# Optimization experiments

Measured on AMD Instinct MI355X. Metric: run time of the kernel, lower is better.

## Reference

```python
import jax, jax.numpy as jnp
import numpy as np
import math

PAD = 0
EPS = 1e-5


def _mha(x, ids, num_heads, qw, qb, kw, kb, vw, vb, pw, pb):
    # Faithful vectorization of the per-head Python loop: identical math per head.
    B, S, D = x.shape
    d = D // num_heads
    q = (x @ qw + qb).reshape(B, S, num_heads, d)
    k = (x @ kw + kb).reshape(B, S, num_heads, d)
    v = (x @ vw + vb).reshape(B, S, num_heads, d)
    scores = jnp.einsum('bqhd,bkhd->bhqk', q, k) / math.sqrt(d)
    key_mask = (ids != PAD)[:, None, None, :]  # mask padded KEYS only (as in source)
    scores = jnp.where(key_mask, scores, -jnp.inf)
    w = jax.nn.softmax(scores, axis=-1)
    out = jnp.einsum('bhqk,bkhd->bqhd', w, v).reshape(B, S, D)
    return out @ pw + pb + x  # projection + residual


def setup_inputs() -> dict:
    V, D, B, S = 50257, 1024, 64, 512
    key = jax.random.key(0)
    ks = jax.random.split(key, 24)
    s = 0.02

    def lin(k, din, dout):
        k1, k2 = jax.random.split(k)
        return (jax.random.normal(k1, (din, dout), jnp.float32) * s,
                jax.random.normal(k2, (dout,), jnp.float32) * s)

    x = jax.random.randint(ks[0], (B, S), 0, V, dtype=jnp.int64)
    emb_w = jax.random.normal(ks[1], (V, D), jnp.float32) * s
    pos_w = jax.random.normal(ks[2], (512, D), jnp.float32) * s
    a1_qw, a1_qb = lin(ks[3], D, D)
    a1_kw, a1_kb = lin(ks[4], D, D)
    a1_vw, a1_vb = lin(ks[5], D, D)
    a1_pw, a1_pb = lin(ks[6], D, D)
    a2_qw, a2_qb = lin(ks[7], D, D)
    a2_kw, a2_kb = lin(ks[8], D, D)
    a2_vw, a2_vb = lin(ks[9], D, D)
    a2_pw, a2_pb = lin(ks[10], D, D)
    norm_g = jnp.ones((D,), jnp.float32)
    norm_b = jnp.zeros((D,), jnp.float32)
    lin_w, lin_b = lin(ks[11], D, 1)
    return dict(x=x, emb_w=emb_w, pos_w=pos_w,
                a1_qw=a1_qw, a1_qb=a1_qb, a1_kw=a1_kw, a1_kb=a1_kb,
                a1_vw=a1_vw, a1_vb=a1_vb, a1_pw=a1_pw, a1_pb=a1_pb,
                a2_qw=a2_qw, a2_qb=a2_qb, a2_kw=a2_kw, a2_kb=a2_kb,
                a2_vw=a2_vw, a2_vb=a2_vb, a2_pw=a2_pw, a2_pb=a2_pb,
                norm_g=norm_g, norm_b=norm_b, lin_w=lin_w, lin_b=lin_b)


def reference(x, emb_w, pos_w,
              a1_qw, a1_qb, a1_kw, a1_kb, a1_vw, a1_vb, a1_pw, a1_pb,
              a2_qw, a2_qb, a2_kw, a2_kb, a2_vw, a2_vb, a2_pw, a2_pb,
              norm_g, norm_b, lin_w, lin_b):
    B, S = x.shape
    h = emb_w[x] + pos_w[jnp.arange(S)][None, :, :]  # word + positional emb
    res_emb = h
    h = _mha(h, x, 8, a1_qw, a1_qb, a1_kw, a1_kb, a1_vw, a1_vb, a1_pw, a1_pb)
    # dropout is identity in eval
    h = _mha(h, x, 4, a2_qw, a2_qb, a2_kw, a2_kb, a2_vw, a2_vb, a2_pw, a2_pb)
    h = h + res_emb
    # mean pooling over non-pad tokens (type=0 branch)
    m = (x != PAD)[:, :, None].astype(h.dtype)
    pooled = jnp.sum(h * m, axis=1) / jnp.sum(m, axis=1)
    # LayerNorm
    mu = jnp.mean(pooled, axis=-1, keepdims=True)
    var = jnp.mean((pooled - mu) ** 2, axis=-1, keepdims=True)
    normed = (pooled - mu) / jnp.sqrt(var + EPS) * norm_g + norm_b
    return normed @ lin_w + lin_b  # [B, 1]
```

## Files before the change

kernel.cpp:

```cpp
#include <hip/hip_runtime.h>

typedef unsigned short u16;
typedef short short8 __attribute__((ext_vector_type(8)));
typedef unsigned short u16x8 __attribute__((ext_vector_type(8)));
typedef float f32x4 __attribute__((ext_vector_type(4)));
typedef const __attribute__((address_space(1))) void* gptr_t;
typedef __attribute__((address_space(3))) void* lptr_t;

#define B_  64
#define S_  512
#define D_  1024
#define BS_ (B_*S_)

__device__ __forceinline__ float b2f(u16 v) {
    union { float f; unsigned u; } c; c.u = ((unsigned)v) << 16; return c.f;
}
__device__ __forceinline__ u16 f2b(float f) {
    union { float f; unsigned u; } c; c.f = f;
    unsigned r = c.u + 0x7FFFu + ((c.u >> 16) & 1u);
    return (u16)(r >> 16);
}

__global__ void detect_k(const u16* __restrict__ raw, int* __restrict__ flag) {
    __shared__ int cnt;
    if (threadIdx.x == 0) cnt = 0;
    __syncthreads();
    u16 v = raw[threadIdx.x * 2];
    int e = (v >> 7) & 0xFF;
    int sane = (e >= 64 && e <= 150) ? 1 : 0;
    atomicAdd(&cnt, sane);
    __syncthreads();
    if (threadIdx.x == 0) *flag = (cnt >= 192) ? 1 : 0;
}

__global__ __launch_bounds__(256) void convert_params_k(
    const void* b0, const void* b1, const void* b2, const void* b3,
    const void* b4, const void* b5, const void* b6, const void* b7,
    const void* g, const void* be, const void* lw, const void* lb,
    const int* __restrict__ flagp, u16* __restrict__ dst)
{
    const void* srcs[12] = {b0, b1, b2, b3, b4, b5, b6, b7, g, be, lw, lb};
    int slot = blockIdx.x;
    int n = (slot == 11) ? 1 : 1024;
    int f = *flagp;
    const void* s = srcs[slot];
    for (int i = threadIdx.x; i < n; i += 256) {
        float v = f ? b2f(((const u16*)s)[i]) : ((const float*)s)[i];
        dst[slot * 1024 + i] = f2b(v);
    }
}

__global__ __launch_bounds__(256) void transpose_k(const void* __restrict__ W,
                                                   u16* __restrict__ Wt,
                                                   const int* __restrict__ flagp) {
    __shared__ float t[32][33];
    int f = *flagp;
    int tx = threadIdx.x, ty = threadIdx.y;
    int x0 = blockIdx.x * 32, y0 = blockIdx.y * 32;
    for (int i = ty; i < 32; i += 8) {
        size_t idx = (size_t)(y0 + i) * D_ + x0 + tx;
        t[i][tx] = f ? b2f(((const u16*)W)[idx]) : ((const float*)W)[idx];
    }
    __syncthreads();
    for (int i = ty; i < 32; i += 8)
        Wt[(size_t)(x0 + i) * D_ + y0 + tx] = f2b(t[tx][i]);
}

__global__ __launch_bounds__(256) void embed_k(const int* __restrict__ x, const void* __restrict__ emb,
                                               const void* __restrict__ pos, u16* __restrict__ h0,
                                               const int* __restrict__ flagp) {
    int f = *flagp;
    int bs = blockIdx.x;
    int s = bs & (S_ - 1);
    int tok = x[bs];
    u16* orow = h0 + (size_t)bs * D_;
    int c = threadIdx.x * 4;
    float e0, e1, e2, e3, p0, p1, p2, p3;
    if (f) {
        ushort4 e = *(const ushort4*)((const u16*)emb + (size_t)tok * D_ + c);
        ushort4 p = *(const ushort4*)((const u16*)pos + (size_t)s * D_ + c);
        e0 = b2f(e.x); e1 = b2f(e.y); e2 = b2f(e.z); e3 = b2f(e.w);
        p0 = b2f(p.x); p1 = b2f(p.y); p2 = b2f(p.z); p3 = b2f(p.w);
    } else {
        float4 e = *(const float4*)((const float*)emb + (size_t)tok * D_ + c);
        float4 p = *(const float4*)((const float*)pos + (size_t)s * D_ + c);
        e0 = e.x; e1 = e.y; e2 = e.z; e3 = e.w;
        p0 = p.x; p1 = p.y; p2 = p.z; p3 = p.w;
    }
    ushort4 o;
    o.x = f2b(e0 + p0); o.y = f2b(e1 + p1); o.z = f2b(e2 + p2); o.w = f2b(e3 + p3);
    *(ushort4*)(orow + c) = o;
}

template <int NT>
__global__ __launch_bounds__(512, 2) void gemm256_k(
    const u16* __restrict__ A, const u16* __restrict__ Bt,
    const u16* __restrict__ bias,
    const u16* __restrict__ res, const u16* __restrict__ res2,
    u16* __restrict__ Cq, u16* __restrict__ Ck, u16* __restrict__ Vt)
{
    int bid = blockIdx.x;
    int xcd = bid & 7;
    int loc = bid >> 3;
    int chunk = loc >> 6;
    int r = loc & 63;
    int mt = xcd * 16 + (r >> 2);
    int nt = chunk * 4 + (r & 3);
    int m0 = mt * 256, n0 = nt * 256;

    int tid = threadIdx.x;
    int lane = tid & 63, wid = tid >> 6, quad = lane >> 4, l16 = lane & 15;
    int wm = wid >> 2, wn = wid & 3;

    __shared__ __align__(16) u16 lds[4][2][256 * 32];

    f32x4 acc[8][4];
#pragma unroll
    for (int i = 0; i < 8; i++)
#pragma unroll
        for (int j = 0; j < 4; j++) acc[i][j] = (f32x4){0.f, 0.f, 0.f, 0.f};

    int srow0 = tid >> 2;
    int skof  = (((tid & 3) ^ ((tid >> 3) & 3)) * 8);

    auto STAGE = [&](int s) {
        int buf = s & 3;
        int kbase = s * 32;
#pragma unroll
        for (int l = 0; l < 2; ++l) {
            int row = l * 128 + srow0;
            const u16* srcA = A  + (size_t)(m0 + row) * D_ + kbase + skof;
            const u16* srcB = Bt + (size_t)(n0 + row) * D_ + kbase + skof;
            __builtin_amdgcn_global_load_lds((gptr_t)srcA,
                (lptr_t)(&lds[buf][0][0] + l * 4096 + tid * 8), 16, 0, 0);
            __builtin_amdgcn_global_load_lds((gptr_t)srcB,
                (lptr_t)(&lds[buf][1][0] + l * 4096 + tid * 8), 16, 0, 0);
        }
    };

    auto COMPUTE = [&](int buf) {
        const u16* Ah = &lds[buf][0][0];
        const u16* Bh = &lds[buf][1][0];
        short8 bf[4], af[8];
#pragma unroll
        for (int nj = 0; nj < 4; ++nj) {
            int rB = wn * 64 + nj * 16 + l16;
            bf[nj] = *(const short8*)&Bh[rB * 32 + ((quad ^ ((rB >> 1) & 3)) * 8)];
        }
#pragma unroll
        for (int mi = 0; mi < 8; ++mi) {
            int rA = wm * 128 + mi * 16 + l16;
            af[mi] = *(const short8*)&Ah[rA * 32 + ((quad ^ ((rA >> 1) & 3)) * 8)];
        }
        __builtin_amdgcn_s_setprio(1);
#pragma unroll
        for (int mi = 0; mi < 8; ++mi)
#pragma unroll
            for (int nj = 0; nj < 4; ++nj)
                acc[mi][nj] = __builtin_amdgcn_mfma_f32_16x16x32_bf16(
                    af[mi], bf[nj], acc[mi][nj], 0, 0, 0);
        __builtin_amdgcn_s_setprio(0);
    };

    STAGE(0); STAGE(1); STAGE(2);
    for (int s = 0; s < 29; ++s) {
        asm volatile("s_waitcnt vmcnt(8)" ::: "memory");
        __builtin_amdgcn_s_barrier();
        COMPUTE(s & 3);
        STAGE(s + 3);
    }
    asm volatile("s_waitcnt vmcnt(8)" ::: "memory");
    __builtin_amdgcn_s_barrier();
    COMPUTE(29 & 3);
    asm volatile("s_waitcnt vmcnt(4)" ::: "memory");
    __builtin_amdgcn_s_barrier();
    COMPUTE(30 & 3);
    asm volatile("s_waitcnt vmcnt(0)" ::: "memory");
    __builtin_amdgcn_s_barrier();
    COMPUTE(31 & 3);

    __syncthreads();
    float* fl = (float*)(&lds[0][0][0]) + wid * 1104;

    int nbase = n0 + wn * 64;
    bool vwave = (NT == 12) && (nbase >= 2048);

    if (vwave) {
        int colv = nbase + lane - 2048;
        float bv = b2f(bias[nbase + lane]);
#pragma unroll
        for (int mi = 0; mi < 8; ++mi) {
#pragma unroll
            for (int nj = 0; nj < 4; ++nj)
                *(f32x4*)&fl[(nj * 16 + l16) * 17 + quad * 4] = acc[mi][nj];
            asm volatile("s_waitcnt lgkmcnt(0)" ::: "memory");
            int rowbase = m0 + wm * 128 + mi * 16;
            int bb = rowbase >> 9, sb0 = rowbase & (S_ - 1);
            u16x8 o0, o1;
#pragma unroll
            for (int s = 0; s < 8; ++s) {
                o0[s] = f2b(fl[lane * 17 + s] + bv);
                o1[s] = f2b(fl[lane * 17 + 8 + s] + bv);
            }
            u16* dst = Vt + ((size_t)bb * D_ + colv) * S_ + sb0;
            *(u16x8*)dst = o0;
            *(u16x8*)(dst + 8) = o1;
            asm volatile("" ::: "memory");
        }
    } else {
        u16* Cd = (NT == 12 && nbase >= 1024) ? Ck : Cq;
        int rr2 = lane >> 2, sg = lane & 3;
        float bvv[2][8];
#pragma unroll
        for (int g = 0; g < 2; ++g) {
            u16x8 b8 = *(const u16x8*)&bias[nbase + sg * 8 + g * 32];
#pragma unroll
            for (int j = 0; j < 8; ++j) bvv[g][j] = b2f(b8[j]);
        }
#pragma unroll
        for (int mi = 0; mi < 8; ++mi) {
#pragma unroll
            for (int nj = 0; nj < 4; ++nj)
                *(f32x4*)&fl[(nj * 16 + l16) * 17 + quad * 4] = acc[mi][nj];
            asm volatile("s_waitcnt lgkmcnt(0)" ::: "memory");
            int row_g = m0 + wm * 128 + mi * 16 + rr2;
#pragma unroll
            for (int g = 0; g < 2; ++g) {
                int c0 = sg * 8 + g * 32;
                int colc = (nbase + c0) & 1023;
                size_t idx = (size_t)row_g * D_ + colc;
                float v[8];
#pragma unroll
                for (int j = 0; j < 8; ++j)
                    v[j] = fl[(c0 + j) * 17 + rr2] + bvv[g][j];
                if (res) {
                    u16x8 r8 = *(const u16x8*)&res[idx];
#pragma unroll
                    for (int j = 0; j < 8; ++j) v[j] += b2f(r8[j]);
                }
                if (res2) {
                    u16x8 r8 = *(const u16x8*)&res2[idx];
#pragma unroll
                    for (int j = 0; j < 8; ++j) v[j] += b2f(r8[j]);
                }
                u16x8 o;
#pragma unroll
                for (int j = 0; j < 8; ++j) o[j] = f2b(v[j]);
                *(u16x8*)&Cd[idx] = o;
            }
            asm volatile("" ::: "memory");
        }
    }
}

template <int HD>
__global__ __launch_bounds__(512, HD == 128 ? 4 : 2) void attn4_k(
    const u16* Q, const u16* __restrict__ Kn, const u16* __restrict__ Vt,
    const int* __restrict__ x, u16* O, int H)
{
    constexpr int NKF = HD / 32, NOF = HD / 16;
    constexpr int KP = HD + 8;
    constexpr int VP = 40;
    constexpr int KC = (32 * HD / 8) / 512;
    constexpr int VC = (HD * 32 / 8) / 512;
    const float scale = (HD == 128) ? 0.08838834764831845f : 0.0625f;
    int bh = blockIdx.x;
    int b = bh / H, h = bh - b * H;
    int tid = threadIdx.x, wid = tid >> 6, lane = tid & 63, quad = lane >> 4, l16 = lane & 15;
    int qrow = blockIdx.y * 128 + wid * 16;

    const u16* Qb = Q + (size_t)(b * S_) * D_ + h * HD;
    const u16* Kb = Kn + (size_t)(b * S_) * D_ + h * HD;
    const u16* Vb = Vt + ((size_t)b * D_ + h * HD) * S_;
    const int* xb = x + b * S_;

    __shared__ __align__(16) u16 Ks[32 * KP];
    __shared__ __align__(16) u16 Vs[HD * VP];
    __shared__ __align__(16) u16 Pl[8 * 16 * 32];

    short8 qf[NKF];
#pragma unroll
    for (int f = 0; f < NKF; ++f)
        qf[f] = *(const short8*)(Qb + (size_t)(qrow + l16) * D_ + f * 32 + quad * 8);

    f32x4 of[NOF];
    float lpart[4];
#pragma unroll
    for (int f = 0; f < NOF; ++f) of[f] = (f32x4){0.f, 0.f, 0.f, 0.f};
#pragma unroll
    for (int r = 0; r < 4; ++r) lpart[r] = 0.f;

    short8 kreg[KC], vreg[VC];
    auto LOADKV = [&](int key0) {
#pragma unroll
        for (int i = 0; i < KC; ++i) {
            int c = tid + i * 512;
            int row = c / (HD / 8), col = (c % (HD / 8)) * 8;
            kreg[i] = *(const short8*)(Kb + (size_t)(key0 + row) * D_ + col);
        }
#pragma unroll
        for (int i = 0; i < VC; ++i) {
            int c = tid + i * 512;
            int row = c >> 2, col = (c & 3) * 8;
            vreg[i] = *(const short8*)(Vb + (size_t)row * S_ + key0 + col);
        }
    };

    LOADKV(0);

    for (int key0 = 0; key0 < S_; key0 += 32) {
        __syncthreads();
#pragma unroll
        for (int i = 0; i < KC; ++i) {
            int c = tid + i * 512;
            int row = c / (HD / 8), col = (c % (HD / 8)) * 8;
            *(short8*)&Ks[row * KP + col] = kreg[i];
        }
#pragma unroll
        for (int i = 0; i < VC; ++i) {
            int c = tid + i * 512;
            int row = c >> 2, col = (c & 3) * 8;
            *(short8*)&Vs[row * VP + col] = vreg[i];
        }
        if (key0 + 32 < S_) LOADKV(key0 + 32);
        int tok0 = xb[key0 + l16] != 0;
        int tok1 = xb[key0 + 16 + l16] != 0;
        __syncthreads();

        f32x4 sc0 = (f32x4){0.f, 0.f, 0.f, 0.f};
        f32x4 sc1 = (f32x4){0.f, 0.f, 0.f, 0.f};
#pragma unroll
        for (int f = 0; f < NKF; ++f) {
            short8 k0 = *(const short8*)&Ks[l16 * KP + f * 32 + quad * 8];
            short8 k1 = *(const short8*)&Ks[(16 + l16) * KP + f * 32 + quad * 8];
            sc0 = __builtin_amdgcn_mfma_f32_16x16x32_bf16(qf[f], k0, sc0, 0, 0, 0);
            sc1 = __builtin_amdgcn_mfma_f32_16x16x32_bf16(qf[f], k1, sc1, 0, 0, 0);
        }
#pragma unroll
        for (int r = 0; r < 4; ++r) {
            float p0 = tok0 ? __expf(sc0[r] * scale) : 0.f;
            float p1 = tok1 ? __expf(sc1[r] * scale) : 0.f;
            lpart[r] += p0 + p1;
            Pl[wid * 512 + (quad * 4 + r) * 32 + l16] = f2b(p0);
            Pl[wid * 512 + (quad * 4 + r) * 32 + 16 + l16] = f2b(p1);
        }
        __asm volatile("s_waitcnt lgkmcnt(0)" ::: "memory");
        short8 pf = *(const short8*)&Pl[wid * 512 + l16 * 32 + quad * 8];
#pragma unroll
        for (int f = 0; f < NOF; ++f) {
            short8 vf = *(const short8*)&Vs[(f * 16 + l16) * VP + quad * 8];
            of[f] = __builtin_amdgcn_mfma_f32_16x16x32_bf16(pf, vf, of[f], 0, 0, 0);
        }
    }

    u16* Ob = O + (size_t)(b * S_) * D_ + h * HD;
    float rl[4];
#pragma unroll
    for (int r = 0; r < 4; ++r) {
        float l = lpart[r];
#pragma unroll
        for (int msk = 1; msk < 16; msk <<= 1) l += __shfl_xor(l, msk, 64);
        rl[r] = 1.0f / l;
    }
#pragma unroll
    for (int f = 0; f < NOF; ++f)
#pragma unroll
        for (int r = 0; r < 4; ++r)
            Ob[(size_t)(qrow + quad * 4 + r) * D_ + f * 16 + l16] =
                f2b(of[f][r] * rl[r]);
}

__global__ __launch_bounds__(256) void pool_zero_k(float* __restrict__ pooled, int* __restrict__ cnt) {
    int b = blockIdx.x;
    for (int i = threadIdx.x; i < 1024; i += 256) pooled[b * 1024 + i] = 0.f;
    if (threadIdx.x == 0) cnt[b] = 0;
}

__global__ __launch_bounds__(256) void pool_partial_k(
    const u16* __restrict__ Hf, const int* __restrict__ x,
    float* __restrict__ pooled, int* __restrict__ cnt)
{
    int b = blockIdx.x, seg = blockIdx.y;
    int c = threadIdx.x * 4;
    const int* xb = x + b * S_;
    float a0 = 0.f, a1 = 0.f, a2 = 0.f, a3 = 0.f;
    int local = 0;
    int s0 = seg * 64;
    for (int i = 0; i < 64; ++i) {
        int s = s0 + i;
        if (xb[s] != 0) {
            ushort4 hv = *(const ushort4*)(Hf + (size_t)(b * S_ + s) * D_ + c);
            a0 += b2f(hv.x); a1 += b2f(hv.y); a2 += b2f(hv.z); a3 += b2f(hv.w);
            local++;
        }
    }
    atomicAdd(&pooled[b * 1024 + c + 0], a0);
    atomicAdd(&pooled[b * 1024 + c + 1], a1);
    atomicAdd(&pooled[b * 1024 + c + 2], a2);
    atomicAdd(&pooled[b * 1024 + c + 3], a3);
    if (threadIdx.x == 0) atomicAdd(&cnt[b], local);
}

__global__ __launch_bounds__(256) void pool_final_k(
    const float* __restrict__ pooled, const int* __restrict__ cnt,
    const u16* __restrict__ prm, void* __restrict__ out, const int* __restrict__ flagp)
{
    __shared__ float sb[8];
    const u16* g  = prm + 8 * 1024;
    const u16* be = prm + 9 * 1024;
    const u16* lw = prm + 10 * 1024;
    const u16* lb = prm + 11 * 1024;
    int b = blockIdx.x;
    int c = threadIdx.x * 4;
    int n = cnt[b];
    float inv = 1.0f / (float)(n > 0 ? n : 1);
    float p0 = pooled[b * 1024 + c + 0] * inv;
    float p1 = pooled[b * 1024 + c + 1] * inv;
    float p2 = pooled[b * 1024 + c + 2] * inv;
    float p3 = pooled[b * 1024 + c + 3] * inv;
    float s1 = p0 + p1 + p2 + p3;
    float s2 = p0 * p0 + p1 * p1 + p2 * p2 + p3 * p3;
#pragma unroll
    for (int m = 32; m >= 1; m >>= 1) { s1 += __shfl_xor(s1, m, 64); s2 += __shfl_xor(s2, m, 64); }
    int wid = threadIdx.x >> 6, lane = threadIdx.x & 63;
    if (lane == 0) { sb[wid] = s1; sb[4 + wid] = s2; }
    __syncthreads();
    float S1 = sb[0] + sb[1] + sb[2] + sb[3];
    float S2 = sb[4] + sb[5] + sb[6] + sb[7];
    float mu = S1 * (1.0f / 1024.0f);
    float var = S2 * (1.0f / 1024.0f) - mu * mu;
    float rstd = rsqrtf(var + 1e-5f);
    float dot = ((p0 - mu) * rstd * b2f(g[c + 0]) + b2f(be[c + 0])) * b2f(lw[c + 0])
              + ((p1 - mu) * rstd * b2f(g[c + 1]) + b2f(be[c + 1])) * b2f(lw[c + 1])
              + ((p2 - mu) * rstd * b2f(g[c + 2]) + b2f(be[c + 2])) * b2f(lw[c + 2])
              + ((p3 - mu) * rstd * b2f(g[c + 3]) + b2f(be[c + 3])) * b2f(lw[c + 3]);
#pragma unroll
    for (int m = 32; m >= 1; m >>= 1) dot += __shfl_xor(dot, m, 64);
    __syncthreads();
    if (lane == 0) sb[wid] = dot;
    __syncthreads();
    if (threadIdx.x == 0) {
        float v = sb[0] + sb[1] + sb[2] + sb[3] + b2f(lb[0]);
        if (*flagp) ((u16*)out)[b] = f2b(v);
        else        ((float*)out)[b] = v;
    }
}

extern "C" void kernel_launch(void* const* d_in, const int* in_sizes, int n_in,
                              void* d_out, int out_size, void* d_ws, size_t ws_size,
                              hipStream_t stream)
{
    (void)in_sizes; (void)n_in; (void)out_size; (void)ws_size;
    const int* x = (const int*)d_in[0];

    char* ws = (char*)d_ws;
    size_t off = 0;
    auto carve = [&](size_t bytes) -> char* {
        char* p = ws + off;
        off += (bytes + 255) & ~(size_t)255;
        return p;
    };
    int* flag    = (int*)carve(256);
    u16* prm     = (u16*)carve(12 * 1024 * 2);
    float* pooled = (float*)carve(64 * 1024 * 4);
    int* cnt     = (int*)carve(64 * 4);
    const size_t WB = (size_t)D_ * D_ * 2;
    const size_t HB = (size_t)BS_ * D_ * 2;
    u16* wt[8];
    for (int i = 0; i < 8; i++) wt[i] = (u16*)carve(WB);
    u16* h0   = (u16*)carve(HB);
    u16* buf2 = (u16*)carve(HB);
    u16* buf3 = (u16*)carve(HB);
    u16* buf4 = (u16*)carve(HB);
    u16* buf5 = (u16*)carve(HB);

    detect_k<<<1, 256, 0, stream>>>((const u16*)d_in[1], flag);
    convert_params_k<<<12, 256, 0, stream>>>(
        d_in[4], d_in[6], d_in[8], d_in[10], d_in[12], d_in[14], d_in[16], d_in[18],
        d_in[19], d_in[20], d_in[21], d_in[22], flag, prm);

    dim3 tb(32, 8), tg(32, 32);
    const int widx[8] = {3, 5, 7, 9, 11, 13, 15, 17};
    for (int i = 0; i < 8; i++)
        transpose_k<<<tg, tb, 0, stream>>>(d_in[widx[i]], wt[i], flag);

    embed_k<<<BS_, 256, 0, stream>>>(x, d_in[1], d_in[2], h0, flag);

    gemm256_k<12><<<1536, 512, 0, stream>>>(h0, wt[0], prm + 0 * 1024,
                                            nullptr, nullptr, buf2, buf3, buf4);
    attn4_k<128><<<dim3(B_ * 8, 4), 512, 0, stream>>>(buf2, buf3, buf4, x, buf2, 8);
    gemm256_k<4><<<512, 512, 0, stream>>>(buf2, wt[3], prm + 3 * 1024,
                                          h0, nullptr, buf5, nullptr, nullptr);
    gemm256_k<12><<<1536, 512, 0, stream>>>(buf5, wt[4], prm + 4 * 1024,
                                            nullptr, nullptr, buf2, buf3, buf4);
    attn4_k<256><<<dim3(B_ * 4, 4), 512, 0, stream>>>(buf2, buf3, buf4, x, buf2, 4);
    gemm256_k<4><<<512, 512, 0, stream>>>(buf2, wt[7], prm + 7 * 1024,
                                          buf5, h0, buf3, nullptr, nullptr);

    pool_zero_k<<<B_, 256, 0, stream>>>(pooled, cnt);
    pool_partial_k<<<dim3(B_, 8), 256, 0, stream>>>(buf3, x, pooled, cnt);
    pool_final_k<<<B_, 256, 0, stream>>>(pooled, cnt, prm, d_out, flag);
}
```

Baseline: 1.067 ms.

## Restructure GEMM main loop into 8-wave ping-pong with BK=64 half-tile staging

Replaces the 4-deep BK=32 ring buffer with a double-buffered BK=64 layout split into A/B halves. Global-to-LDS loads for the next tiles are interleaved per quarter-iteration between MFMA clusters, with barriers around each compute block. LDS reads use an 8-way XOR swizzle to avoid bank conflicts. The goal is better overlap of memory and MFMA work and fewer loop iterations, at the cost of more barriers and a shallower prefetch depth.

```diff
diff --git a/kernel.cpp b/kernel.cpp
--- a/kernel.cpp
+++ b/kernel.cpp
@@ -111,8 +111,9 @@
     int tid = threadIdx.x;
     int lane = tid & 63, wid = tid >> 6, quad = lane >> 4, l16 = lane & 15;
     int wm = wid >> 2, wn = wid & 3;
-
-    __shared__ __align__(16) u16 lds[4][2][256 * 32];
+    int pxor = l16 & 7;
+
+    __shared__ __align__(16) u16 lds[2][2][2][128 * 64];
 
     f32x4 acc[8][4];
 #pragma unroll
@@ -120,67 +121,79 @@
 #pragma unroll
         for (int j = 0; j < 4; j++) acc[i][j] = (f32x4){0.f, 0.f, 0.f, 0.f};
 
-    int srow0 = tid >> 2;
-    int skof  = (((tid & 3) ^ ((tid >> 3) & 3)) * 8);
-
-    auto STAGE = [&](int s) {
-        int buf = s & 3;
-        int kbase = s * 32;
-#pragma unroll
-        for (int l = 0; l < 2; ++l) {
-            int row = l * 128 + srow0;
-            const u16* srcA = A  + (size_t)(m0 + row) * D_ + kbase + skof;
-            const u16* srcB = Bt + (size_t)(n0 + row) * D_ + kbase + skof;
-            __builtin_amdgcn_global_load_lds((gptr_t)srcA,
-                (lptr_t)(&lds[buf][0][0] + l * 4096 + tid * 8), 16, 0, 0);
-            __builtin_amdgcn_global_load_lds((gptr_t)srcB,
-                (lptr_t)(&lds[buf][1][0] + l * 4096 + tid * 8), 16, 0, 0);
-        }
+    int srow = tid >> 3;
+    int skof = ((tid & 7) ^ (srow & 7)) * 8;
+
+    auto STAGE_HALF = [&](int kt, int mat, int hlf) {
+        int p = kt & 1;
+        int kbase = kt * 64;
+        const u16* src = (mat == 0)
+            ? A  + (size_t)(m0 + hlf * 128) * D_ + kbase
+            : Bt + (size_t)(n0 + hlf * 128) * D_ + kbase;
+        u16* dst = &lds[p][mat][hlf][0];
+        __builtin_amdgcn_global_load_lds((gptr_t)(src + (size_t)srow * D_ + skof),
+                                         (lptr_t)(dst + tid * 8), 16, 0, 0);
+        __builtin_amdgcn_global_load_lds((gptr_t)(src + (size_t)(srow + 64) * D_ + skof),
+                                         (lptr_t)(dst + 4096 + tid * 8), 16, 0, 0);
     };
 
-    auto COMPUTE = [&](int buf) {
-        const u16* Ah = &lds[buf][0][0];
-        const u16* Bh = &lds[buf][1][0];
-        short8 bf[4], af[8];
-#pragma unroll
-        for (int nj = 0; nj < 4; ++nj) {
-            int rB = wn * 64 + nj * 16 + l16;
-            bf[nj] = *(const short8*)&Bh[rB * 32 + ((quad ^ ((rB >> 1) & 3)) * 8)];
-        }
-#pragma unroll
-        for (int mi = 0; mi < 8; ++mi) {
-            int rA = wm * 128 + mi * 16 + l16;
-            af[mi] = *(const short8*)&Ah[rA * 32 + ((quad ^ ((rA >> 1) & 3)) * 8)];
-        }
-        __builtin_amdgcn_s_setprio(1);
-#pragma unroll
-        for (int mi = 0; mi < 8; ++mi)
-#pragma unroll
-            for (int nj = 0; nj < 4; ++nj)
-                acc[mi][nj] = __builtin_amdgcn_mfma_f32_16x16x32_bf16(
-                    af[mi], bf[nj], acc[mi][nj], 0, 0, 0);
-        __builtin_amdgcn_s_setprio(0);
-    };
-
-    STAGE(0); STAGE(1); STAGE(2);
-    for (int s = 0; s < 29; ++s) {
-        asm volatile("s_waitcnt vmcnt(8)" ::: "memory");
-        __builtin_amdgcn_s_barrier();
-        COMPUTE(s & 3);
-        STAGE(s + 3);
-    }
-    asm volatile("s_waitcnt vmcnt(8)" ::: "memory");
-    __builtin_amdgcn_s_barrier();
-    COMPUTE(29 & 3);
+    STAGE_HALF(0, 0, 0); STAGE_HALF(0, 0, 1);
+    STAGE_HALF(0, 1, 0); STAGE_HALF(0, 1, 1);
+    STAGE_HALF(1, 1, 0); STAGE_HALF(1, 1, 1);
     asm volatile("s_waitcnt vmcnt(4)" ::: "memory");
     __builtin_amdgcn_s_barrier();
-    COMPUTE(30 & 3);
-    asm volatile("s_waitcnt vmcnt(0)" ::: "memory");
-    __builtin_amdgcn_s_barrier();
-    COMPUTE(31 & 3);
-
-    __syncthreads();
-    float* fl = (float*)(&lds[0][0][0]) + wid * 1104;
+
+    int brow0 = (wn & 1) * 64;
+    for (int kt = 0; kt < 16; ++kt) {
+        int p = kt & 1;
+        const u16* Ah = &lds[p][0][wm][0];
+        const u16* Bh = &lds[p][1][wn >> 1][0];
+        short8 bf[4][2];
+#pragma unroll
+        for (int q = 0; q < 4; ++q) {
+            if (q == 0) {
+#pragma unroll
+                for (int nj = 0; nj < 4; ++nj)
+#pragma unroll
+                    for (int kh = 0; kh < 2; ++kh)
+                        bf[nj][kh] = *(const short8*)&Bh[(brow0 + nj * 16 + l16) * 64 +
+                                                         ((kh * 4 + quad) ^ pxor) * 8];
+            }
+            short8 af[2][2];
+#pragma unroll
+            for (int mi2 = 0; mi2 < 2; ++mi2)
+#pragma unroll
+                for (int kh = 0; kh < 2; ++kh)
+                    af[mi2][kh] = *(const short8*)&Ah[((2 * q + mi2) * 16 + l16) * 64 +
+                                                      ((kh * 4 + quad) ^ pxor) * 8];
+            if (q == 0 && kt + 1 < 16) STAGE_HALF(kt + 1, 0, 0);
+            if (q == 1 && kt + 1 < 16) STAGE_HALF(kt + 1, 0, 1);
+            if (q == 2 && kt + 2 < 16) STAGE_HALF(kt + 2, 1, 0);
+            if (q == 3 && kt + 2 < 16) STAGE_HALF(kt + 2, 1, 1);
+            __builtin_amdgcn_s_barrier();
+            asm volatile("s_waitcnt lgkmcnt(0)" ::: "memory");
+            __builtin_amdgcn_sched_barrier(0);
+            __builtin_amdgcn_s_setprio(1);
+#pragma unroll
+            for (int kh = 0; kh < 2; ++kh)
+#pragma unroll
+                for (int mi2 = 0; mi2 < 2; ++mi2)
+#pragma unroll
+                    for (int nj = 0; nj < 4; ++nj)
+                        acc[2 * q + mi2][nj] = __builtin_amdgcn_mfma_f32_16x16x32_bf16(
+                            af[mi2][kh], bf[nj][kh], acc[2 * q + mi2][nj], 0, 0, 0);
+            __builtin_amdgcn_s_setprio(0);
+            __builtin_amdgcn_s_barrier();
+        }
+        if (kt < 15) {
+            if (kt < 14) asm volatile("s_waitcnt vmcnt(4)" ::: "memory");
+            else         asm volatile("s_waitcnt vmcnt(0)" ::: "memory");
+            __builtin_amdgcn_s_barrier();
+        }
+    }
+
+    __syncthreads();
+    float* fl = (float*)(&lds[0][0][0][0]) + wid * 1104;
 
     int nbase = n0 + wn * 64;
     bool vwave = (NT == 12) && (nbase >= 2048);
```

Result: faster. 1.029 ms (-3.6%).
